# Kernel tuning notes

Measured on AMD Instinct MI355X. Metric: run time of the kernel, lower is better.

## Reference

```python
import jax, jax.numpy as jnp
import numpy as np

N = 4096  # number of rows == cols (init arg N)
D = 64    # point feature dimension


def setup_inputs() -> dict:
    key = jax.random.key(0)
    kx, ky = jax.random.split(key)
    return {
        "xINP": jax.random.normal(kx, (N, D), dtype=jnp.float32),
        "yINP": jax.random.normal(ky, (N, D), dtype=jnp.float32),
    }


def _pairwise_euclidean(x, y):
    # scipy.spatial.distance_matrix default p=2: sqrt(sum((xi - yj)^2))
    sq = (jnp.sum(x * x, axis=1)[:, None]
          + jnp.sum(y * y, axis=1)[None, :]
          - 2.0 * (x @ y.T))
    return jnp.sqrt(jnp.maximum(sq, 0.0))  # [N, N]


def _greedy_match(cost):
    # Greedy bipartite matching: visit all (i, j) pairs in ascending cost
    # order; accept a pair iff both row i and col j are still unmatched.
    n, m = cost.shape
    order = jnp.argsort(cost.reshape(-1))          # stable sort, like python sorted
    rows = (order // m).astype(jnp.int32)          # [n*m]
    cols = (order % m).astype(jnp.int32)           # [n*m]

    def step(carry, ij):
        rm, cm = carry
        i, j = ij
        free = (rm[i] == -1) & (cm[j] == -1)
        rm = rm.at[i].set(jnp.where(free, j, rm[i]))
        cm = cm.at[j].set(jnp.where(free, i, cm[j]))
        return (rm, cm), None

    init = (jnp.full((n,), -1, dtype=jnp.int32),   # row_to_col_match_vec
            jnp.full((m,), -1, dtype=jnp.int32))   # col_to_row_match_vec
    (_, cm), _ = jax.lax.scan(step, init, (rows, cols))
    return cm


def reference(xINP, yINP):
    cost = _pairwise_euclidean(xINP, yINP)   # [N, N]
    return _greedy_match(cost)               # [N] int32: col_to_row_match_vec
```

## Files before the change

### kernel.cpp

```cpp
#include <hip/hip_runtime.h>
#include <stdint.h>

#define NN 4096
#define DD 64
#define GCOL 16
#define CCH 16
#define RCHK 8
#define TMAX 112
#define TGMAX 512
#define NROUNDS 20
#define ROUNDS_FB 32

typedef unsigned long long u64;
typedef unsigned int u32;

#define RESC 0xFFFFFFFFFFFFFFFEull
#define EMPTY (~0ull)

__device__ __forceinline__ u64 pk(float d, u32 idx) {
  return (((u64)__float_as_uint(d)) << 32) | (u64)idx;
}

__device__ __forceinline__ float distfly(const float* __restrict__ x,
                                         const float* __restrict__ y,
                                         float xxi, float yyj, int i, int j) {
  const float* xi = x + (size_t)i * DD;
  const float* yj = y + (size_t)j * DD;
  float dot = 0.f;
#pragma unroll
  for (int k = 0; k < DD; ++k) dot = fmaf(xi[k], yj[k], dot);
  float sq = (xxi + yyj) - 2.0f * dot;
  return sqrtf(fmaxf(sq, 0.f));
}

__global__ void k_init(const float* __restrict__ x, const float* __restrict__ y,
                       float* xx, float* yy, int* rm, int* cm, int* FR, int* Fcnt,
                       u64* rowbest, u64* rowpart, u64* colpart) {
  int i = blockIdx.x * blockDim.x + threadIdx.x;
  if (i < NN) {
    const float* xi = x + (size_t)i * DD;
    const float* yi = y + (size_t)i * DD;
    float sx = 0.f, sy = 0.f;
#pragma unroll
    for (int k = 0; k < DD; ++k) { sx = fmaf(xi[k], xi[k], sx); sy = fmaf(yi[k], yi[k], sy); }
    xx[i] = sx; yy[i] = sy;
    rm[i] = -1; cm[i] = -1; FR[i] = i;
    rowbest[i] = EMPTY;
#pragma unroll
    for (int h = 0; h < RCHK; ++h) rowpart[(size_t)h * NN + i] = RESC;
#pragma unroll
    for (int g = 0; g < CCH; ++g) colpart[(size_t)g * NN + i] = RESC;
    if (i == 0) *Fcnt = NN;
  }
}

__global__ void k_build(const float* __restrict__ x, const float* __restrict__ y,
                        const float* __restrict__ xx, const float* __restrict__ yy,
                        float* __restrict__ C) {
  __shared__ float xs[64][65];
  __shared__ float ys[64][65];
  int t = threadIdx.x;
  int bi = blockIdx.y * 64, bj = blockIdx.x * 64;
  for (int e = t; e < 64 * 64; e += 256) {
    int r = e >> 6, c = e & 63;
    xs[r][c] = x[(size_t)(bi + r) * DD + c];
    ys[r][c] = y[(size_t)(bj + r) * DD + c];
  }
  __syncthreads();
  int tx = t & 15, ty = t >> 4;
  float acc[4][4];
#pragma unroll
  for (int r = 0; r < 4; ++r)
#pragma unroll
    for (int c = 0; c < 4; ++c) acc[r][c] = 0.f;
#pragma unroll
  for (int k = 0; k < 64; ++k) {
    float a[4], b[4];
#pragma unroll
    for (int r = 0; r < 4; ++r) a[r] = xs[ty * 4 + r][k];
#pragma unroll
    for (int c = 0; c < 4; ++c) b[c] = ys[tx * 4 + c][k];
#pragma unroll
    for (int r = 0; r < 4; ++r)
#pragma unroll
      for (int c = 0; c < 4; ++c) acc[r][c] = fmaf(a[r], b[c], acc[r][c]);
  }
#pragma unroll
  for (int r = 0; r < 4; ++r) {
    int i = bi + ty * 4 + r;
    float xxi = xx[i];
    float4 v;
    float* vp = (float*)&v;
#pragma unroll
    for (int c = 0; c < 4; ++c) {
      int j = bj + tx * 4 + c;
      float sq = (xxi + yy[j]) - 2.0f * acc[r][c];
      vp[c] = sqrtf(fmaxf(sq, 0.f));
    }
    *(float4*)(C + (size_t)i * NN + bj + tx * 4) = v;
  }
}

__global__ void k_round2(const float* __restrict__ C, const int* __restrict__ rm,
                         const int* __restrict__ cm, u64* __restrict__ rowbest,
                         u64* __restrict__ rowpart, u64* __restrict__ colpart) {
  __shared__ u64 red[256];
  __shared__ u64 rp[RCHK];
  __shared__ int stale[RCHK];
  __shared__ u64 part[4][64];
  int b = blockIdx.x;
  int t = threadIdx.x;
  if (b < NN) {
    int i = b;
    if (rm[i] != -1) return;
    u64 rb = rowbest[i];
    u32 jb = (u32)rb;
    if (jb < NN && cm[jb] == -1) return;
    if (t < RCHK) {
      u64 e = rowpart[(size_t)t * NN + i];
      rp[t] = e;
      u32 je = (u32)e;
      stale[t] = (e != EMPTY) && !(je < NN && cm[je] == -1);
    }
    __syncthreads();
    const float* Ci = C + (size_t)i * NN;
    for (int h = 0; h < RCHK; ++h) {
      if (!stale[h]) continue;
      int j0 = h * 512 + t * 2;
      float2 v = *(const float2*)(Ci + j0);
      int2 m = *(const int2*)(cm + j0);
      u64 best = EMPTY;
      if (m.x == -1) best = pk(v.x, (u32)j0);
      if (m.y == -1) { u64 k2 = pk(v.y, (u32)(j0 + 1)); if (k2 < best) best = k2; }
      red[t] = best;
      __syncthreads();
      for (int s = 128; s > 0; s >>= 1) {
        if (t < s) { if (red[t + s] < red[t]) red[t] = red[t + s]; }
        __syncthreads();
      }
      if (t == 0) { rp[h] = red[0]; rowpart[(size_t)h * NN + i] = red[0]; }
      __syncthreads();
    }
    if (t == 0) {
      u64 best = rp[0];
#pragma unroll
      for (int h = 1; h < RCHK; ++h) if (rp[h] < best) best = rp[h];
      rowbest[i] = best;
    }
  } else {
    int idx = b - NN;
    int cb = idx & 63, g = idx >> 6;
    int lane = t & 63, s = t >> 6;
    int j = cb * 64 + lane;
    u64* slot = colpart + (size_t)g * NN + j;
    bool stale_c = false;
    if (cm[j] == -1) {
      u64 e = *slot;
      if (e != EMPTY) { u32 io = (u32)e; stale_c = !(io < NN && rm[io] == -1); }
    }
    u64 best = EMPTY;
    if (stale_c) {
      int i0 = g * 256 + s * 64;
      for (int i = i0; i < i0 + 64; ++i) {
        if (rm[i] != -1) continue;
        u64 key = pk(C[(size_t)i * NN + j], (u32)i);
        if (key < best) best = key;
      }
    }
    part[s][lane] = best;
    __syncthreads();
    if (s == 0 && stale_c) {
      u64 b0 = part[0][lane];
#pragma unroll
      for (int q = 1; q < 4; ++q) if (part[q][lane] < b0) b0 = part[q][lane];
      *slot = b0;
    }
  }
}

__global__ void k_accept3(const u64* __restrict__ colpart, const u64* __restrict__ rowbest,
                          int* rm, int* cm, int* Fcnt) {
  if (*Fcnt == 0) return;
  int j = blockIdx.x * 256 + threadIdx.x;
  if (cm[j] != -1) return;
  u64 best = EMPTY;
#pragma unroll
  for (int g = 0; g < CCH; ++g) {
    u64 v = colpart[(size_t)g * NN + j];
    if (v < best) best = v;
  }
  u32 io = (u32)best;
  if (io >= NN) return;
  int i = (int)io;
  if (rm[i] == -1 && (u32)(rowbest[i] & 0xffffffffu) == (u32)j) {
    rm[i] = j; cm[j] = i;
    atomicSub(Fcnt, 1);
  }
}

__global__ __launch_bounds__(256) void k_endgame(const float* __restrict__ C,
                                                 int* rm, int* cm, int* FRg,
                                                 float* __restrict__ G) {
  __shared__ __align__(16) char shb[54272];
  int* sFR5 = (int*)shb;
  int* sFC5 = (int*)(shb + 2048);
  float* Csub = (float*)(shb + 4096);
  u64* rkey2 = (u64*)(shb + 4096);
  int* rcol2 = (int*)(shb + 8192);
  int* cfree2 = (int*)(shb + 10240);
  int* dl = (int*)(shb + 12288);
  __shared__ int sF, sG, sc_star, scnt;
  __shared__ u64 rkey[TMAX];
  __shared__ int rcol[TMAX];
  __shared__ int cfree[TMAX];
  __shared__ u64 wred[4];
  __shared__ u64 red[256];
  __shared__ int redi[256];
  int t = threadIdx.x;
  if (t == 0) { sF = 0; sG = 0; }
  __syncthreads();
  for (int i = t; i < NN; i += 256)
    if (rm[i] == -1) { int p = atomicAdd(&sF, 1); if (p < TGMAX) sFR5[p] = i; }
  for (int j = t; j < NN; j += 256)
    if (cm[j] == -1) { int p = atomicAdd(&sG, 1); if (p < TGMAX) sFC5[p] = j; }
  __syncthreads();
  int F = sF;
  if (F == 0) return;
  if (F <= TMAX) {
    for (int r = (t >> 6); r < F; r += 4) {
      const float* Ci = C + (size_t)sFR5[r] * NN;
      for (int c = (t & 63); c < F; c += 64) Csub[r * F + c] = Ci[sFC5[c]];
    }
    for (int c = t; c < F; c += 256) cfree[c] = 1;
    __syncthreads();
    for (int r = t; r < F; r += 256) {
      const float* row = Csub + r * F;
      u64 bk = ~0ull; int bc = 0; int ig = sFR5[r];
      for (int c = 0; c < F; ++c) {
        u64 k = (((u64)__float_as_uint(row[c])) << 24) | (u32)(ig * NN + sFC5[c]);
        if (k < bk) { bk = k; bc = c; }
      }
      rkey[r] = bk; rcol[r] = bc;
    }
    __syncthreads();
    for (int it = 0; it < F; ++it) {
      u64 kb = ~0ull;
      if (t < F && rkey[t] != ~0ull) kb = (rkey[t] << 8) | (u64)(u32)t;
      for (int s = 32; s > 0; s >>= 1) {
        u64 o = __shfl_down(kb, s, 64);
        if (o < kb) kb = o;
      }
      if ((t & 63) == 0) wred[t >> 6] = kb;
      __syncthreads();
      if (t == 0) {
        u64 bmin = wred[0];
#pragma unroll
        for (int wv = 1; wv < 4; ++wv) if (wred[wv] < bmin) bmin = wred[wv];
        int rstar = (int)(bmin & 255);
        if (rstar >= F) rstar = 0;
        int cstar = rcol[rstar];
        sc_star = cstar;
        int i = sFR5[rstar], j = sFC5[cstar];
        rm[i] = j; cm[j] = i;
        rkey[rstar] = ~0ull; cfree[cstar] = 0;
      }
      __syncthreads();
      int cs = sc_star;
      for (int r = t; r < F; r += 256) {
        if (rkey[r] != ~0ull && rcol[r] == cs) {
          const float* row = Csub + r * F;
          u64 bk = ~0ull; int bc = 0; int ig = sFR5[r];
          for (int c = 0; c < F; ++c) {
            if (!cfree[c]) continue;
            u64 k = (((u64)__float_as_uint(row[c])) << 24) | (u32)(ig * NN + sFC5[c]);
            if (k < bk) { bk = k; bc = c; }
          }
          rkey[r] = bk; rcol[r] = bc;
        }
      }
      __syncthreads();
    }
  } else if (F <= TGMAX && G != nullptr) {
    for (int r = (t >> 6); r < F; r += 4) {
      const float* Ci = C + (size_t)sFR5[r] * NN;
      for (int c = (t & 63); c < F; c += 64) G[(size_t)r * F + c] = Ci[sFC5[c]];
    }
    for (int c = t; c < F; c += 256) cfree2[c] = 1;
    __syncthreads();
    for (int r = t; r < F; r += 256) {
      const float* row = G + (size_t)r * F;
      u64 bk = ~0ull; int bc = 0; int ig = sFR5[r];
      for (int c = 0; c < F; ++c) {
        u64 k = (((u64)__float_as_uint(row[c])) << 24) | (u32)(ig * NN + sFC5[c]);
        if (k < bk) { bk = k; bc = c; }
      }
      rkey2[r] = bk; rcol2[r] = bc;
    }
    __syncthreads();
    for (int it = 0; it < F; ++it) {
      u64 lv = ~0ull; int la = 0;
      for (int r = t; r < F; r += 256)
        if (rkey2[r] < lv) { lv = rkey2[r]; la = r; }
      red[t] = lv; redi[t] = la;
      __syncthreads();
      for (int s = 128; s > 0; s >>= 1) {
        if (t < s && red[t + s] < red[t]) { red[t] = red[t + s]; redi[t] = redi[t + s]; }
        __syncthreads();
      }
      if (t == 0) {
        int rstar = redi[0];
        int cstar = rcol2[rstar];
        sc_star = cstar;
        rm[sFR5[rstar]] = sFC5[cstar]; cm[sFC5[cstar]] = sFR5[rstar];
        rkey2[rstar] = ~0ull; cfree2[cstar] = 0;
        scnt = 0;
      }
      __syncthreads();
      int cs = sc_star;
      for (int r = t; r < F; r += 256)
        if (rkey2[r] != ~0ull && rcol2[r] == cs) { int p = atomicAdd(&scnt, 1); dl[p] = r; }
      __syncthreads();
      int nd = scnt;
      for (int d = 0; d < nd; ++d) {
        int r = dl[d];
        const float* Gr = G + (size_t)r * F;
        int ig = sFR5[r];
        u64 lb = ~0ull; int lc = 0;
        for (int c = t; c < F; c += 256) {
          if (!cfree2[c]) continue;
          u64 k = (((u64)__float_as_uint(Gr[c])) << 24) | (u32)(ig * NN + sFC5[c]);
          if (k < lb) { lb = k; lc = c; }
        }
        red[t] = lb; redi[t] = lc;
        __syncthreads();
        for (int s = 128; s > 0; s >>= 1) {
          if (t < s && red[t + s] < red[t]) { red[t] = red[t + s]; redi[t] = redi[t + s]; }
          __syncthreads();
        }
        if (t == 0) { rkey2[r] = red[0]; rcol2[r] = redi[0]; }
        __syncthreads();
      }
    }
  } else {
    for (int it = 0; it < NN; ++it) {
      if (t == 0) scnt = 0;
      __syncthreads();
      for (int i = t; i < NN; i += 256)
        if (rm[i] == -1) { int p = atomicAdd(&scnt, 1); FRg[p] = i; }
      __syncthreads();
      int Fa = scnt;
      if (Fa == 0) break;
      u64 best = ~0ull;
      int total = Fa * NN;
      for (int idx = t; idx < total; idx += 256) {
        int bb2 = idx >> 12, j = idx & 4095;
        if (cm[j] != -1) continue;
        int i = FRg[bb2];
        u64 key = pk(C[(size_t)i * NN + j], (u32)(i * NN + j));
        if (key < best) best = key;
      }
      red[t] = best;
      __syncthreads();
      for (int s = 128; s > 0; s >>= 1) {
        if (t < s) { if (red[t + s] < red[t]) red[t] = red[t + s]; }
        __syncthreads();
      }
      if (t == 0) {
        u32 lo = (u32)red[0];
        rm[lo >> 12] = lo & 4095; cm[lo & 4095] = lo >> 12;
      }
      __syncthreads();
    }
  }
}

template <bool USEC>
__global__ void k_rowpass(const float* __restrict__ C,
                          const float* __restrict__ x, const float* __restrict__ y,
                          const float* __restrict__ xx, const float* __restrict__ yy,
                          const int* __restrict__ cm, const int* __restrict__ FR,
                          const int* __restrict__ Fcnt, u64* __restrict__ rowbest) {
  int b = blockIdx.x;
  if (b >= *Fcnt) return;
  int i = FR[b];
  __shared__ float xsh[DD];
  __shared__ u64 red[256];
  int t = threadIdx.x;
  if (!USEC) { if (t < DD) xsh[t] = x[(size_t)i * DD + t]; }
  __syncthreads();
  float xxi = xx[i];
  u64 best = ~0ull;
  for (int j = t; j < NN; j += 256) {
    if (cm[j] != -1) continue;
    float d;
    if (USEC) {
      d = C[(size_t)i * NN + j];
    } else {
      const float* yj = y + (size_t)j * DD;
      float dot = 0.f;
#pragma unroll
      for (int k = 0; k < DD; ++k) dot = fmaf(xsh[k], yj[k], dot);
      float sq = (xxi + yy[j]) - 2.0f * dot;
      d = sqrtf(fmaxf(sq, 0.f));
    }
    u64 key = pk(d, (u32)j);
    if (key < best) best = key;
  }
  red[t] = best;
  __syncthreads();
  for (int s = 128; s > 0; s >>= 1) {
    if (t < s) { if (red[t + s] < red[t]) red[t] = red[t + s]; }
    __syncthreads();
  }
  if (t == 0) rowbest[i] = red[0];
}

template <bool USEC>
__global__ void k_colpass(const float* __restrict__ C,
                          const float* __restrict__ x, const float* __restrict__ y,
                          const float* __restrict__ xx, const float* __restrict__ yy,
                          const int* __restrict__ cm, const int* __restrict__ FR,
                          const int* __restrict__ Fcnt, u64* __restrict__ colpart) {
  int t = threadIdx.x;
  int j = blockIdx.x * 256 + t;
  int g = blockIdx.y;
  int F = *Fcnt;
  if (F == 0) return;
  int b0 = (g * F) / GCOL, b1 = ((g + 1) * F) / GCOL;
  u64 best = ~0ull;
  if (cm[j] == -1) {
    float yyj = yy[j];
    if (USEC) {
      for (int b = b0; b < b1; ++b) {
        int i = FR[b];
        u64 key = pk(C[(size_t)i * NN + j], (u32)i);
        if (key < best) best = key;
      }
    } else {
      float4 yr[16];
      const float4* yj4 = (const float4*)(y + (size_t)j * DD);
#pragma unroll
      for (int q = 0; q < 16; ++q) yr[q] = yj4[q];
      for (int b = b0; b < b1; ++b) {
        int i = FR[b];
        const float4* xi4 = (const float4*)(x + (size_t)i * DD);
        float dot = 0.f;
#pragma unroll
        for (int q = 0; q < 16; ++q) {
          float4 a = xi4[q], bb = yr[q];
          dot = fmaf(a.x, bb.x, dot); dot = fmaf(a.y, bb.y, dot);
          dot = fmaf(a.z, bb.z, dot); dot = fmaf(a.w, bb.w, dot);
        }
        float sq = (xx[i] + yyj) - 2.0f * dot;
        float d = sqrtf(fmaxf(sq, 0.f));
        u64 key = pk(d, (u32)i);
        if (key < best) best = key;
      }
    }
  }
  colpart[(size_t)g * NN + j] = best;
}

__global__ void k_accept(const u64* __restrict__ colpart, const u64* __restrict__ rowbest,
                         int* rm, int* cm, int* FR, int* Fcnt) {
  __shared__ int scnt;
  int t = threadIdx.x;
  if (*Fcnt == 0) return;
  for (int j = t; j < NN; j += 1024) {
    if (cm[j] != -1) continue;
    u64 best = ~0ull;
#pragma unroll
    for (int g = 0; g < GCOL; ++g) {
      u64 v = colpart[(size_t)g * NN + j];
      if (v < best) best = v;
    }
    u32 io = (u32)best;
    if (io >= NN) continue;
    int i = (int)io;
    if (rm[i] == -1 && (u32)(rowbest[i] & 0xffffffffu) == (u32)j) { rm[i] = j; cm[j] = i; }
  }
  __syncthreads();
  if (t == 0) scnt = 0;
  __syncthreads();
  for (int i = t; i < NN; i += 1024)
    if (rm[i] == -1) { int p = atomicAdd(&scnt, 1); FR[p] = i; }
  __syncthreads();
  if (t == 0) *Fcnt = scnt;
}

template <bool USEC>
__global__ void k_cleanup(const float* __restrict__ C,
                          const float* __restrict__ x, const float* __restrict__ y,
                          const float* __restrict__ xx, const float* __restrict__ yy,
                          int* rm, int* cm, int* FR) {
  __shared__ int scnt;
  __shared__ u64 red[1024];
  int t = threadIdx.x;
  for (int it = 0; it < NN; ++it) {
    if (t == 0) scnt = 0;
    __syncthreads();
    for (int i = t; i < NN; i += 1024)
      if (rm[i] == -1) { int p = atomicAdd(&scnt, 1); FR[p] = i; }
    __syncthreads();
    int F = scnt;
    if (F == 0) break;
    u64 best = ~0ull;
    int total = F * NN;
    for (int idx = t; idx < total; idx += 1024) {
      int b = idx >> 12;
      int j = idx & 4095;
      if (cm[j] != -1) continue;
      int i = FR[b];
      float d;
      if (USEC) d = C[(size_t)i * NN + j];
      else d = distfly(x, y, xx[i], yy[j], i, j);
      u64 key = pk(d, (u32)(i * NN + j));
      if (key < best) best = key;
    }
    red[t] = best;
    __syncthreads();
    for (int s = 512; s > 0; s >>= 1) {
      if (t < s) { if (red[t + s] < red[t]) red[t] = red[t + s]; }
      __syncthreads();
    }
    if (t == 0) {
      u32 lo = (u32)red[0];
      int i = lo >> 12, j = lo & 4095;
      rm[i] = j; cm[j] = i;
    }
    __syncthreads();
  }
}

extern "C" void kernel_launch(void* const* d_in, const int* in_sizes, int n_in,
                              void* d_out, int out_size, void* d_ws, size_t ws_size,
                              hipStream_t stream) {
  const float* x = (const float*)d_in[0];
  const float* y = (const float*)d_in[1];
  int* cm = (int*)d_out;

  char* w = (char*)d_ws;
  float* xx = (float*)(w + 0);
  float* yy = (float*)(w + 16384);
  int* rm = (int*)(w + 32768);
  int* FR = (int*)(w + 49152);
  int* Fcnt = (int*)(w + 65536);
  u64* rowbest = (u64*)(w + 65664);
  u64* rowpart = (u64*)(w + 98432);
  u64* colpart = (u64*)(w + 360704);
  float* C = (float*)(w + 1048576);
  float* G = (float*)(w + 68157440);

  size_t need_c = 1048576 + (size_t)NN * NN * 4;
  size_t need_g = 68157440 + (size_t)TGMAX * TGMAX * 4;
  bool usec = ws_size >= need_c;
  bool useg = ws_size >= need_g;

  k_init<<<dim3(16), 256, 0, stream>>>(x, y, xx, yy, rm, cm, FR, Fcnt,
                                       rowbest, rowpart, colpart);
  if (usec) {
    k_build<<<dim3(64, 64), 256, 0, stream>>>(x, y, xx, yy, C);
    for (int r = 0; r < NROUNDS; ++r) {
      k_round2<<<dim3(NN + 64 * CCH), 256, 0, stream>>>(C, rm, cm, rowbest, rowpart, colpart);
      k_accept3<<<dim3(16), 256, 0, stream>>>(colpart, rowbest, rm, cm, Fcnt);
    }
    k_endgame<<<dim3(1), 256, 0, stream>>>(C, rm, cm, FR, useg ? G : nullptr);
  } else {
    for (int r = 0; r < ROUNDS_FB; ++r) {
      k_rowpass<false><<<dim3(NN), 256, 0, stream>>>(nullptr, x, y, xx, yy, cm, FR, Fcnt, rowbest);
      k_colpass<false><<<dim3(16, GCOL), 256, 0, stream>>>(nullptr, x, y, xx, yy, cm, FR, Fcnt, colpart);
      k_accept<<<dim3(1), 1024, 0, stream>>>(colpart, rowbest, rm, cm, FR, Fcnt);
    }
    k_cleanup<false><<<dim3(1), 1024, 0, stream>>>(nullptr, x, y, xx, yy, rm, cm, FR);
  }
}
```

Before: 674.0 us.

## Rescan stale row chunks per-wavefront with shuffle reductions, fewer rounds

Each stale 512-column row chunk is now rescanned by a single wavefront, which uses vectorized float4/int4 loads and a 64-lane shuffle min reduction instead of a block-wide shared-memory tree. The four wavefronts cover two chunks each, and one final cross-wave min runs through shared memory. This removes the per-chunk __syncthreads chains and serial chunk iteration. The fixed round count NROUNDS also drops from 20 to 17, which shifts work toward the fallback path.

```diff
diff --git a/kernel.cpp b/kernel.cpp
--- a/kernel.cpp
+++ b/kernel.cpp
@@ -8,7 +8,7 @@
 #define RCHK 8
 #define TMAX 112
 #define TGMAX 512
-#define NROUNDS 20
+#define NROUNDS 17
 #define ROUNDS_FB 32
 
 typedef unsigned long long u64;
@@ -104,53 +104,62 @@
 __global__ void k_round2(const float* __restrict__ C, const int* __restrict__ rm,
                          const int* __restrict__ cm, u64* __restrict__ rowbest,
                          u64* __restrict__ rowpart, u64* __restrict__ colpart) {
-  __shared__ u64 red[256];
-  __shared__ u64 rp[RCHK];
-  __shared__ int stale[RCHK];
+  __shared__ u64 wbest[4];
   __shared__ u64 part[4][64];
   int b = blockIdx.x;
   int t = threadIdx.x;
+  int lane = t & 63, w = t >> 6;
   if (b < NN) {
     int i = b;
     if (rm[i] != -1) return;
     u64 rb = rowbest[i];
     u32 jb = (u32)rb;
     if (jb < NN && cm[jb] == -1) return;
-    if (t < RCHK) {
-      u64 e = rowpart[(size_t)t * NN + i];
-      rp[t] = e;
+    const float* Ci = C + (size_t)i * NN;
+    u64 mycv = EMPTY;
+#pragma unroll
+    for (int pass = 0; pass < 2; ++pass) {
+      int h = w + pass * 4;
+      u64 e = rowpart[(size_t)h * NN + i];
       u32 je = (u32)e;
-      stale[t] = (e != EMPTY) && !(je < NN && cm[je] == -1);
-    }
-    __syncthreads();
-    const float* Ci = C + (size_t)i * NN;
-    for (int h = 0; h < RCHK; ++h) {
-      if (!stale[h]) continue;
-      int j0 = h * 512 + t * 2;
-      float2 v = *(const float2*)(Ci + j0);
-      int2 m = *(const int2*)(cm + j0);
-      u64 best = EMPTY;
-      if (m.x == -1) best = pk(v.x, (u32)j0);
-      if (m.y == -1) { u64 k2 = pk(v.y, (u32)(j0 + 1)); if (k2 < best) best = k2; }
-      red[t] = best;
-      __syncthreads();
-      for (int s = 128; s > 0; s >>= 1) {
-        if (t < s) { if (red[t + s] < red[t]) red[t] = red[t + s]; }
-        __syncthreads();
-      }
-      if (t == 0) { rp[h] = red[0]; rowpart[(size_t)h * NN + i] = red[0]; }
-      __syncthreads();
-    }
+      bool stale = (e != EMPTY) && !(je < NN && cm[je] == -1);
+      u64 cv = e;
+      if (stale) {
+        int j0 = h * 512 + lane * 8;
+        float4 v0 = *(const float4*)(Ci + j0);
+        float4 v1 = *(const float4*)(Ci + j0 + 4);
+        int4 m0 = *(const int4*)(cm + j0);
+        int4 m1 = *(const int4*)(cm + j0 + 4);
+        const float* vp0 = (const float*)&v0; const int* mp0 = (const int*)&m0;
+        const float* vp1 = (const float*)&v1; const int* mp1 = (const int*)&m1;
+        u64 bl = EMPTY;
+#pragma unroll
+        for (int c = 0; c < 4; ++c)
+          if (mp0[c] == -1) { u64 k2 = pk(vp0[c], (u32)(j0 + c)); if (k2 < bl) bl = k2; }
+#pragma unroll
+        for (int c = 0; c < 4; ++c)
+          if (mp1[c] == -1) { u64 k2 = pk(vp1[c], (u32)(j0 + 4 + c)); if (k2 < bl) bl = k2; }
+#pragma unroll
+        for (int md = 1; md < 64; md <<= 1) {
+          u64 o = __shfl_xor(bl, md, 64);
+          if (o < bl) bl = o;
+        }
+        cv = bl;
+        if (lane == 0) rowpart[(size_t)h * NN + i] = bl;
+      }
+      if (cv < mycv) mycv = cv;
+    }
+    if (lane == 0) wbest[w] = mycv;
+    __syncthreads();
     if (t == 0) {
-      u64 best = rp[0];
-#pragma unroll
-      for (int h = 1; h < RCHK; ++h) if (rp[h] < best) best = rp[h];
+      u64 best = wbest[0];
+#pragma unroll
+      for (int w2 = 1; w2 < 4; ++w2) if (wbest[w2] < best) best = wbest[w2];
       rowbest[i] = best;
     }
   } else {
     int idx = b - NN;
     int cb = idx & 63, g = idx >> 6;
-    int lane = t & 63, s = t >> 6;
     int j = cb * 64 + lane;
     u64* slot = colpart + (size_t)g * NN + j;
     bool stale_c = false;
@@ -160,16 +169,16 @@
     }
     u64 best = EMPTY;
     if (stale_c) {
-      int i0 = g * 256 + s * 64;
+      int i0 = g * 256 + w * 64;
       for (int i = i0; i < i0 + 64; ++i) {
         if (rm[i] != -1) continue;
         u64 key = pk(C[(size_t)i * NN + j], (u32)i);
         if (key < best) best = key;
       }
     }
-    part[s][lane] = best;
-    __syncthreads();
-    if (s == 0 && stale_c) {
+    part[w][lane] = best;
+    __syncthreads();
+    if (w == 0 && stale_c) {
       u64 b0 = part[0][lane];
 #pragma unroll
       for (int q = 1; q < 4; ++q) if (part[q][lane] < b0) b0 = part[q][lane];
```

After: 731.3 us. 8.5% more time.
